# Performance work log

Hardware: AMD Instinct MI355X
Metric: run time of the kernel (lower is better)

Reference implementation:

```python
import jax, jax.numpy as jnp
import numpy as np

ODE_UNFOLDS = 6          # kerasncp LTCCell default
EPS = 1e-8               # kerasncp LTCCell epsilon


def _masks(d):
    """Adjacency masks from MemoryCellWiring: self-synapses on all 2d units,
    cross synapses src<->src+d (polarity -1); sensory src->src and src->src+d
    (polarity +1)."""
    units = 2 * d
    m = np.eye(units, dtype=np.float32)
    m[:d, d:] += np.eye(d, dtype=np.float32)
    m[d:, :d] += np.eye(d, dtype=np.float32)
    sm = np.zeros((d, units), dtype=np.float32)
    sm[:, :d] = np.eye(d, dtype=np.float32)
    sm[:, d:] = np.eye(d, dtype=np.float32)
    return jnp.asarray(m), jnp.asarray(sm)


def setup_inputs() -> dict:
    key = jax.random.key(0)
    B, T, d = 32, 128, 128
    units = 2 * d
    ks = jax.random.split(key, 12)
    U = lambda k, shp, lo, hi: jax.random.uniform(k, shp, jnp.float32, lo, hi)
    mask, smask = _masks(d)
    return {
        "inputs": jax.random.normal(ks[0], (B, T, d), jnp.float32),
        # affine input/output mappings (kerasncp init: ones / zeros)
        "input_w": jnp.ones((d,), jnp.float32),
        "input_b": jnp.zeros((d,), jnp.float32),
        "output_w": jnp.ones((d,), jnp.float32),
        "output_b": jnp.zeros((d,), jnp.float32),
        # per-neuron params (kerasncp init ranges)
        "gleak": U(ks[1], (units,), 0.001, 1.0),
        "vleak": U(ks[2], (units,), -0.2, 0.2),
        "cm": U(ks[3], (units,), 0.4, 0.6),
        # recurrent synapse params (units, units); erev initialized to polarity
        "w": U(ks[4], (units, units), 0.001, 1.0),
        "mu": U(ks[5], (units, units), 0.3, 0.8),
        "sigma": U(ks[6], (units, units), 3.0, 8.0),
        "erev": -mask,
        # sensory synapse params (d, units); polarity +1
        "sensory_w": U(ks[7], (d, units), 0.001, 1.0),
        "sensory_mu": U(ks[8], (d, units), 0.3, 0.8),
        "sensory_sigma": U(ks[9], (d, units), 3.0, 8.0),
        "sensory_erev": smask,
    }


def reference(inputs, input_w, input_b, output_w, output_b,
              gleak, vleak, cm, w, mu, sigma, erev,
              sensory_w, sensory_mu, sensory_sigma, sensory_erev):
    B, T, d = inputs.shape
    units = 2 * d
    mask, smask = _masks(d)
    x = inputs * input_w + input_b          # affine input mapping, (B,T,d)
    cm_t = cm * ODE_UNFOLDS                  # cm / (elapsed_time / ode_unfolds), elapsed=1

    def step(v, x_t):
        # sensory activations, computed once per timestep: (B, d, units)
        sa = sensory_w * jax.nn.sigmoid((x_t[:, :, None] - sensory_mu) * sensory_sigma) * smask
        wnum_s = jnp.sum(sa * sensory_erev, axis=1)   # (B, units)
        wden_s = jnp.sum(sa, axis=1)                  # (B, units)

        def unfold(v, _):
            # semi-implicit Euler fixed-point step; (B, units, units)
            wa = w * jax.nn.sigmoid((v[:, :, None] - mu) * sigma) * mask
            num = cm_t * v + gleak * vleak + jnp.sum(wa * erev, axis=1) + wnum_s
            den = cm_t + gleak + jnp.sum(wa, axis=1) + wden_s
            return num / (den + EPS), None

        v, _ = jax.lax.scan(unfold, v, None, length=ODE_UNFOLDS)
        return v, None

    v0 = jnp.zeros((B, units), inputs.dtype)
    vT, _ = jax.lax.scan(step, v0, jnp.swapaxes(x, 0, 1))
    # motor neurons = first output_dim = d units, then affine output mapping
    return vT[:, :d] * output_w + output_b
```

## Files before the change

### kernel.cpp

```cpp
#include <hip/hip_runtime.h>

#define ODE_UNFOLDS 6
#define LTC_EPS 1e-8f


__device__ __forceinline__ float swap_pair(float x) {
    return __int_as_float(
        __builtin_amdgcn_mov_dpp(__float_as_int(x), 0xB1, 0xF, 0xF, true));
}

__global__ __launch_bounds__(64)
void ltc_lane_kernel(const float* __restrict__ inputs,
                     const float* __restrict__ input_w, const float* __restrict__ input_b,
                     const float* __restrict__ output_w, const float* __restrict__ output_b,
                     const float* __restrict__ gleak, const float* __restrict__ vleak,
                     const float* __restrict__ cm,
                     const float* __restrict__ w, const float* __restrict__ mu,
                     const float* __restrict__ sigma, const float* __restrict__ erev,
                     const float* __restrict__ sw, const float* __restrict__ smu,
                     const float* __restrict__ ssig, const float* __restrict__ serev,
                     float* __restrict__ out,
                     int B, int T, int d)
{
    const int tid = blockIdx.x * blockDim.x + threadIdx.x;
    const int units = 2 * d;
    if (tid >= B * units) return;

    const int pairIdx = tid >> 1;
    const int h = tid & 1;
    const int b = pairIdx / d;
    const int j = pairIdx - b * d;
    const int u  = j + h * d;
    const int pu = j + (1 - h) * d;

    const float LOG2E = 1.4426950408889634f;

    float A_s, C_s, W_s, WE_s, A_c, C_c, W_c, WE_c;
    {
        int i = u * units + u;
        float sg = sigma[i], m = mu[i];
        A_s = -sg * LOG2E; C_s = m * sg * LOG2E; W_s = w[i]; WE_s = W_s * erev[i];
        i = pu * units + u;
        sg = sigma[i]; m = mu[i];
        A_c = -sg * LOG2E; C_c = m * sg * LOG2E; W_c = w[i]; WE_c = W_c * erev[i];
    }

    float siA, siC, sW, sWE;
    {
        int i = j * units + u;
        float sg = ssig[i], m = smu[i];
        float sA = -sg * LOG2E, sC = m * sg * LOG2E;
        const float iw = input_w[j], ib = input_b[j];
        siA = iw * sA; siC = ib * sA + sC;
        sW = sw[i]; sWE = sW * serev[i];
    }

    const float cmu = cm[u] * (float)ODE_UNFOLDS;
    const float gl  = gleak[u];
    const float gv  = gl * vleak[u];
    const float den0 = cmu + gl + LTC_EPS;

    const float* __restrict__ xin = inputs + (size_t)b * T * d + j;

    float v = 0.f;

    const int TU = 4;
    float xbuf[TU];
#pragma unroll
    for (int k = 0; k < TU; ++k) xbuf[k] = xin[(size_t)k * d];

    for (int g = 0; g < T; g += TU) {
        float xnext[TU];
        if (g + TU < T) {
#pragma unroll
            for (int k = 0; k < TU; ++k) xnext[k] = xin[(size_t)(g + TU + k) * d];
        } else {
#pragma unroll
            for (int k = 0; k < TU; ++k) xnext[k] = 0.f;
        }

#pragma unroll
        for (int k = 0; k < TU; ++k) {
            const float es = __builtin_amdgcn_exp2f(fmaf(xbuf[k], siA, siC));
            const float ss = __builtin_amdgcn_rcpf(1.f + es);
            const float nb = fmaf(sWE, ss, gv);
            const float db = fmaf(sW,  ss, den0);

#pragma unroll
            for (int uu = 0; uu < ODE_UNFOLDS; ++uu) {
                const float vp = swap_pair(v);
                const float ea = __builtin_amdgcn_exp2f(fmaf(v,  A_s, C_s));
                const float eb = __builtin_amdgcn_exp2f(fmaf(vp, A_c, C_c));
                const float a  = 1.f + ea;
                const float bb = 1.f + eb;
                const float r  = __builtin_amdgcn_rcpf(a * bb);
                const float s_s = r * bb;
                const float s_c = r * a;

                float num = fmaf(cmu, v, nb);
                num = fmaf(WE_s, s_s, num);
                num = fmaf(WE_c, s_c, num);
                float den = fmaf(W_s, s_s, db);
                den = fmaf(W_c, s_c, den);

                v = num * __builtin_amdgcn_rcpf(den);
            }
        }

#pragma unroll
        for (int k = 0; k < TU; ++k) xbuf[k] = xnext[k];
    }

    if (h == 0) {
        out[(size_t)b * d + j] = fmaf(v, output_w[j], output_b[j]);
    }
}

extern "C" void kernel_launch(void* const* d_in, const int* in_sizes, int n_in,
                              void* d_out, int out_size, void* d_ws, size_t ws_size,
                              hipStream_t stream) {
    const float* inputs   = (const float*)d_in[0];
    const float* input_w  = (const float*)d_in[1];
    const float* input_b  = (const float*)d_in[2];
    const float* output_w = (const float*)d_in[3];
    const float* output_b = (const float*)d_in[4];
    const float* gleak    = (const float*)d_in[5];
    const float* vleak    = (const float*)d_in[6];
    const float* cm       = (const float*)d_in[7];
    const float* w        = (const float*)d_in[8];
    const float* mu       = (const float*)d_in[9];
    const float* sigma    = (const float*)d_in[10];
    const float* erev     = (const float*)d_in[11];
    const float* sw       = (const float*)d_in[12];
    const float* smu      = (const float*)d_in[13];
    const float* ssig     = (const float*)d_in[14];
    const float* serev    = (const float*)d_in[15];
    float* out = (float*)d_out;

    const int d = in_sizes[1];
    const int B = out_size / d;
    const int T = in_sizes[0] / (B * d);

    const int total = B * 2 * d;
    const int block = 64;
    const int grid = (total + block - 1) / block;
    ltc_lane_kernel<<<grid, block, 0, stream>>>(
        inputs, input_w, input_b, output_w, output_b,
        gleak, vleak, cm, w, mu, sigma, erev,
        sw, smu, ssig, serev, out, B, T, d);
}
```

Baseline: 43.67 us.

## Restructure LTC unfold recurrence to merge reciprocals and shorten dependency chain

Rewrites each ODE unfold step algebraically. Both sigmoid denominators are multiplied through into a single numerator/denominator pair, so each step needs only one reciprocal, and v is carried implicitly as num*r. Each lane now computes the cross-synapse exponential its partner needs, using the transposed mu/sigma entry, and exchanges the result through DPP after the exp instead of swapping v before it. This is meant to shorten the serial latency chain per unfold, at the cost of a few extra FMAs and possibly different rounding or overflow behaviour in the products of exponentials.

After: 43.57 us. About the same (-0.2%).

```diff
diff --git a/kernel.cpp b/kernel.cpp
--- a/kernel.cpp
+++ b/kernel.cpp
@@ -35,15 +35,26 @@
 
     const float LOG2E = 1.4426950408889634f;
 
-    float A_s, C_s, W_s, WE_s, A_c, C_c, W_c, WE_c;
+    float A_s, C_s, W_s, WE_s;
     {
         int i = u * units + u;
         float sg = sigma[i], m = mu[i];
-        A_s = -sg * LOG2E; C_s = m * sg * LOG2E; W_s = w[i]; WE_s = W_s * erev[i];
-        i = pu * units + u;
-        sg = sigma[i]; m = mu[i];
-        A_c = -sg * LOG2E; C_c = m * sg * LOG2E; W_c = w[i]; WE_c = W_c * erev[i];
+        A_s = -sg * LOG2E; C_s = m * sg * LOG2E;
+        W_s = w[i]; WE_s = W_s * erev[i];
     }
+    float W_c, WE_c;
+    {
+        int i = pu * units + u;
+        W_c = w[i]; WE_c = W_c * erev[i];
+    }
+    float A_o, C_o;
+    {
+        int i = u * units + pu;
+        float sg = sigma[i], m = mu[i];
+        A_o = -sg * LOG2E; C_o = m * sg * LOG2E;
+    }
+    const float Wsum  = W_s + W_c;
+    const float WEsum = WE_s + WE_c;
 
     float siA, siC, sW, sWE;
     {
@@ -62,7 +73,7 @@
 
     const float* __restrict__ xin = inputs + (size_t)b * T * d + j;
 
-    float v = 0.f;
+    float num = 0.f, r = 1.f;
 
     const int TU = 4;
     float xbuf[TU];
@@ -81,29 +92,39 @@
 
 #pragma unroll
         for (int k = 0; k < TU; ++k) {
-            const float es = __builtin_amdgcn_exp2f(fmaf(xbuf[k], siA, siC));
-            const float ss = __builtin_amdgcn_rcpf(1.f + es);
-            const float nb = fmaf(sWE, ss, gv);
-            const float db = fmaf(sW,  ss, den0);
+            const float es_ = __builtin_amdgcn_exp2f(fmaf(xbuf[k], siA, siC));
+            const float ss  = __builtin_amdgcn_rcpf(1.f + es_);
+            const float nb  = fmaf(sWE, ss, gv);
+            const float db  = fmaf(sW,  ss, den0);
+            const float K0  = db + Wsum;
+            const float Ks  = db + W_c;
+            const float Kx  = db + W_s;
 
 #pragma unroll
             for (int uu = 0; uu < ODE_UNFOLDS; ++uu) {
-                const float vp = swap_pair(v);
-                const float ea = __builtin_amdgcn_exp2f(fmaf(v,  A_s, C_s));
-                const float eb = __builtin_amdgcn_exp2f(fmaf(vp, A_c, C_c));
-                const float a  = 1.f + ea;
-                const float bb = 1.f + eb;
-                const float r  = __builtin_amdgcn_rcpf(a * bb);
-                const float s_s = r * bb;
-                const float s_c = r * a;
+                const float v    = num * r;
+                const float t    = fmaf(cmu, v, nb);
+                const float ts   = A_s * num;
+                const float to   = A_o * num;
+                const float args = fmaf(ts, r, C_s);
+                const float argo = fmaf(to, r, C_o);
+                const float es = __builtin_amdgcn_exp2f(args);
+                const float eo = __builtin_amdgcn_exp2f(argo);
+                const float ex = swap_pair(eo);
 
-                float num = fmaf(cmu, v, nb);
-                num = fmaf(WE_s, s_s, num);
-                num = fmaf(WE_c, s_c, num);
-                float den = fmaf(W_s, s_s, db);
-                den = fmaf(W_c, s_c, den);
+                const float m  = es * ex;
+                float dsum = fmaf(Ks, es, K0);
+                dsum = fmaf(Kx, ex, dsum);
+                dsum = fmaf(db, m, dsum);
 
-                v = num * __builtin_amdgcn_rcpf(den);
+                const float c1 = t + WE_c;
+                const float c2 = t + WE_s;
+                float nsum = fmaf(c1, es, t + WEsum);
+                nsum = fmaf(c2, ex, nsum);
+                nsum = fmaf(t, m, nsum);
+
+                num = nsum;
+                r = __builtin_amdgcn_rcpf(dsum);
             }
         }
 
@@ -112,6 +133,7 @@
     }
 
     if (h == 0) {
+        const float v = num * r;
         out[(size_t)b * d + j] = fmaf(v, output_w[j], output_b[j]);
     }
 }
```

## Compute both coupled neurons per thread and fold sigmoids into rational form

Applied to the files above, without the earlier changes.

Each thread now owns a whole pair of coupled neurons (j and j+d), so the DPP lane swap goes away and half as many threads are launched. The sigmoid terms are rewritten as exp products multiplied through the numerator and denominator, which drops the per-step product reciprocal and leaves one reciprocal per neuron. v is carried as num*r, so the next step's exponent argument can be formed without waiting for the division. This gives more independent work per thread to hide latency on the serial chain, but also halves the wave count (64 waves total) and raises register use.

Result: slower. 73.49 us (+68.3%).

```diff
diff --git a/kernel.cpp b/kernel.cpp
--- a/kernel.cpp
+++ b/kernel.cpp
@@ -4,65 +4,72 @@
 #define LTC_EPS 1e-8f
 
 
-__device__ __forceinline__ float swap_pair(float x) {
-    return __int_as_float(
-        __builtin_amdgcn_mov_dpp(__float_as_int(x), 0xB1, 0xF, 0xF, true));
-}
-
 __global__ __launch_bounds__(64)
-void ltc_lane_kernel(const float* __restrict__ inputs,
-                     const float* __restrict__ input_w, const float* __restrict__ input_b,
-                     const float* __restrict__ output_w, const float* __restrict__ output_b,
-                     const float* __restrict__ gleak, const float* __restrict__ vleak,
-                     const float* __restrict__ cm,
-                     const float* __restrict__ w, const float* __restrict__ mu,
-                     const float* __restrict__ sigma, const float* __restrict__ erev,
-                     const float* __restrict__ sw, const float* __restrict__ smu,
-                     const float* __restrict__ ssig, const float* __restrict__ serev,
-                     float* __restrict__ out,
-                     int B, int T, int d)
+void ltc_pair2_kernel(const float* __restrict__ inputs,
+                      const float* __restrict__ input_w, const float* __restrict__ input_b,
+                      const float* __restrict__ output_w, const float* __restrict__ output_b,
+                      const float* __restrict__ gleak, const float* __restrict__ vleak,
+                      const float* __restrict__ cm,
+                      const float* __restrict__ w, const float* __restrict__ mu,
+                      const float* __restrict__ sigma, const float* __restrict__ erev,
+                      const float* __restrict__ sw, const float* __restrict__ smu,
+                      const float* __restrict__ ssig, const float* __restrict__ serev,
+                      float* __restrict__ out,
+                      int B, int T, int d)
 {
     const int tid = blockIdx.x * blockDim.x + threadIdx.x;
+    if (tid >= B * d) return;
+    const int b = tid / d;
+    const int j = tid - b * d;
     const int units = 2 * d;
-    if (tid >= B * units) return;
-
-    const int pairIdx = tid >> 1;
-    const int h = tid & 1;
-    const int b = pairIdx / d;
-    const int j = pairIdx - b * d;
-    const int u  = j + h * d;
-    const int pu = j + (1 - h) * d;
+    const int p = j + d;
 
     const float LOG2E = 1.4426950408889634f;
 
-    float A_s, C_s, W_s, WE_s, A_c, C_c, W_c, WE_c;
+    float AsA, CsA, WsA, WEsA, AcA, CcA, WcA, WEcA;
     {
-        int i = u * units + u;
+        int i = j * units + j;
         float sg = sigma[i], m = mu[i];
-        A_s = -sg * LOG2E; C_s = m * sg * LOG2E; W_s = w[i]; WE_s = W_s * erev[i];
-        i = pu * units + u;
+        AsA = -sg * LOG2E; CsA = m * sg * LOG2E; WsA = w[i]; WEsA = WsA * erev[i];
+        i = p * units + j;
         sg = sigma[i]; m = mu[i];
-        A_c = -sg * LOG2E; C_c = m * sg * LOG2E; W_c = w[i]; WE_c = W_c * erev[i];
+        AcA = -sg * LOG2E; CcA = m * sg * LOG2E; WcA = w[i]; WEcA = WcA * erev[i];
+    }
+    float AsB, CsB, WsB, WEsB, AcB, CcB, WcB, WEcB;
+    {
+        int i = p * units + p;
+        float sg = sigma[i], m = mu[i];
+        AsB = -sg * LOG2E; CsB = m * sg * LOG2E; WsB = w[i]; WEsB = WsB * erev[i];
+        i = j * units + p;
+        sg = sigma[i]; m = mu[i];
+        AcB = -sg * LOG2E; CcB = m * sg * LOG2E; WcB = w[i]; WEcB = WcB * erev[i];
+    }
+    const float WsumA = WsA + WcA,  WEsumA = WEsA + WEcA;
+    const float WsumB = WsB + WcB,  WEsumB = WEsB + WEcB;
+
+    float siAA, siCA, sWA, sWEA, siAB, siCB, sWB, sWEB;
+    {
+        const float iw = input_w[j], ib = input_b[j];
+        int i = j * units + j;
+        float sg = ssig[i], m = smu[i];
+        float sA = -sg * LOG2E, sC = m * sg * LOG2E;
+        siAA = iw * sA; siCA = ib * sA + sC; sWA = sw[i]; sWEA = sWA * serev[i];
+        i = j * units + p;
+        sg = ssig[i]; m = smu[i];
+        sA = -sg * LOG2E; sC = m * sg * LOG2E;
+        siAB = iw * sA; siCB = ib * sA + sC; sWB = sw[i]; sWEB = sWB * serev[i];
     }
 
-    float siA, siC, sW, sWE;
-    {
-        int i = j * units + u;
-        float sg = ssig[i], m = smu[i];
-        float sA = -sg * LOG2E, sC = m * sg * LOG2E;
-        const float iw = input_w[j], ib = input_b[j];
-        siA = iw * sA; siC = ib * sA + sC;
-        sW = sw[i]; sWE = sW * serev[i];
-    }
-
-    const float cmu = cm[u] * (float)ODE_UNFOLDS;
-    const float gl  = gleak[u];
-    const float gv  = gl * vleak[u];
-    const float den0 = cmu + gl + LTC_EPS;
+    const float cmA = cm[j] * (float)ODE_UNFOLDS;
+    const float cmB = cm[p] * (float)ODE_UNFOLDS;
+    const float glA = gleak[j], glB = gleak[p];
+    const float gvA = glA * vleak[j], gvB = glB * vleak[p];
+    const float den0A = cmA + glA + LTC_EPS;
+    const float den0B = cmB + glB + LTC_EPS;
 
     const float* __restrict__ xin = inputs + (size_t)b * T * d + j;
 
-    float v = 0.f;
+    float numA = 0.f, rA = 1.f, numB = 0.f, rB = 1.f;
 
     const int TU = 4;
     float xbuf[TU];
@@ -81,29 +88,53 @@
 
 #pragma unroll
         for (int k = 0; k < TU; ++k) {
-            const float es = __builtin_amdgcn_exp2f(fmaf(xbuf[k], siA, siC));
-            const float ss = __builtin_amdgcn_rcpf(1.f + es);
-            const float nb = fmaf(sWE, ss, gv);
-            const float db = fmaf(sW,  ss, den0);
+            const float eA_ = __builtin_amdgcn_exp2f(fmaf(xbuf[k], siAA, siCA));
+            const float eB_ = __builtin_amdgcn_exp2f(fmaf(xbuf[k], siAB, siCB));
+            const float ssA = __builtin_amdgcn_rcpf(1.f + eA_);
+            const float ssB = __builtin_amdgcn_rcpf(1.f + eB_);
+            const float nbA = fmaf(sWEA, ssA, gvA);
+            const float dbA = fmaf(sWA,  ssA, den0A);
+            const float nbB = fmaf(sWEB, ssB, gvB);
+            const float dbB = fmaf(sWB,  ssB, den0B);
+            const float K0A = dbA + WsumA, KsA = dbA + WcA, KxA = dbA + WsA;
+            const float K0B = dbB + WsumB, KsB = dbB + WcB, KxB = dbB + WsB;
 
 #pragma unroll
             for (int uu = 0; uu < ODE_UNFOLDS; ++uu) {
-                const float vp = swap_pair(v);
-                const float ea = __builtin_amdgcn_exp2f(fmaf(v,  A_s, C_s));
-                const float eb = __builtin_amdgcn_exp2f(fmaf(vp, A_c, C_c));
-                const float a  = 1.f + ea;
-                const float bb = 1.f + eb;
-                const float r  = __builtin_amdgcn_rcpf(a * bb);
-                const float s_s = r * bb;
-                const float s_c = r * a;
+                const float vA = numA * rA;
+                const float vB = numB * rB;
+                const float tA = fmaf(cmA, vA, nbA);
+                const float tB = fmaf(cmB, vB, nbB);
 
-                float num = fmaf(cmu, v, nb);
-                num = fmaf(WE_s, s_s, num);
-                num = fmaf(WE_c, s_c, num);
-                float den = fmaf(W_s, s_s, db);
-                den = fmaf(W_c, s_c, den);
+                const float argsA = fmaf(AsA * numA, rA, CsA);
+                const float argsB = fmaf(AsB * numB, rB, CsB);
+                const float argcA = fmaf(AcA * numB, rB, CcA);
+                const float argcB = fmaf(AcB * numA, rA, CcB);
 
-                v = num * __builtin_amdgcn_rcpf(den);
+                const float esA = __builtin_amdgcn_exp2f(argsA);
+                const float esB = __builtin_amdgcn_exp2f(argsB);
+                const float ecA = __builtin_amdgcn_exp2f(argcA);
+                const float ecB = __builtin_amdgcn_exp2f(argcB);
+
+                const float mA = esA * ecA;
+                const float mB = esB * ecB;
+
+                float dA = fmaf(KsA, esA, K0A);
+                dA = fmaf(KxA, ecA, dA);
+                dA = fmaf(dbA, mA, dA);
+                float dB = fmaf(KsB, esB, K0B);
+                dB = fmaf(KxB, ecB, dB);
+                dB = fmaf(dbB, mB, dB);
+
+                float nA = fmaf(tA + WEcA, esA, tA + WEsumA);
+                nA = fmaf(tA + WEsA, ecA, nA);
+                nA = fmaf(tA, mA, nA);
+                float nB = fmaf(tB + WEcB, esB, tB + WEsumB);
+                nB = fmaf(tB + WEsB, ecB, nB);
+                nB = fmaf(tB, mB, nB);
+
+                numA = nA; rA = __builtin_amdgcn_rcpf(dA);
+                numB = nB; rB = __builtin_amdgcn_rcpf(dB);
             }
         }
 
@@ -111,9 +142,8 @@
         for (int k = 0; k < TU; ++k) xbuf[k] = xnext[k];
     }
 
-    if (h == 0) {
-        out[(size_t)b * d + j] = fmaf(v, output_w[j], output_b[j]);
-    }
+    const float vA = numA * rA;
+    out[(size_t)b * d + j] = fmaf(vA, output_w[j], output_b[j]);
 }
 
 extern "C" void kernel_launch(void* const* d_in, const int* in_sizes, int n_in,
@@ -141,10 +171,10 @@
     const int B = out_size / d;
     const int T = in_sizes[0] / (B * d);
 
-    const int total = B * 2 * d;
+    const int total = B * d;
     const int block = 64;
     const int grid = (total + block - 1) / block;
-    ltc_lane_kernel<<<grid, block, 0, stream>>>(
+    ltc_pair2_kernel<<<grid, block, 0, stream>>>(
         inputs, input_w, input_b, output_w, output_b,
         gleak, vleak, cm, w, mu, sigma, erev,
         sw, smu, ssig, serev, out, B, T, d);
```
